# Kernel optimization log

Measured on AMD Instinct MI355X. Metric: run time of the kernel, lower is better.

The kernel has to match this reference:

```python
import jax, jax.numpy as jnp
import numpy as np

B, S, H, D = 2, 2048, 16, 128  # batch, seq, n_head, head_dim; n_embd = H*D
N_EMBD = H * D

def setup_inputs() -> dict:
    key = jax.random.key(0)
    kq, kk, kv = jax.random.split(key, 3)
    q = jax.random.normal(kq, (B, S, H, D), dtype=jnp.float32)
    k = jax.random.normal(kk, (B, S, H, D), dtype=jnp.float32)
    v = jax.random.normal(kv, (B, S, H, D), dtype=jnp.float32)
    return {"q": q, "k": k, "v": v}

def reference(q, k, v):
    # [B,S,H,D] -> [B,H,S,D]
    qh = jnp.transpose(q, (0, 2, 1, 3))
    kh = jnp.transpose(k, (0, 2, 1, 3))
    vh = jnp.transpose(v, (0, 2, 1, 3))
    # scores scaled by head_dim (NOT sqrt), matching the original module
    att = jnp.einsum('bhqd,bhkd->bhqk', qh, kh) / D
    att = jax.nn.softmax(att, axis=-1)
    y = jnp.einsum('bhqk,bhkd->bhqd', att, vh)
    # [B,H,S,D] -> [B,S,H,D] -> [B*S, n_embd]
    y = jnp.transpose(y, (0, 2, 1, 3)).reshape(B * S, N_EMBD)
    return y
```

## Files before the change

### kernel.cpp

```cpp
#include <hip/hip_runtime.h>


#define SEQ   2048
#define NHEAD 16
#define DH    128
#define NB    2
#define BQ    256
#define BK    64
#define NTHR  256
#define KSTR  136
#define VSTR  72
#define NKV   (SEQ / BK)
#define NELEM (NB * SEQ * NHEAD * DH)

typedef __attribute__((ext_vector_type(8)))  short bf16x8;
typedef __attribute__((ext_vector_type(16))) float f32x16;
typedef __attribute__((ext_vector_type(4)))  unsigned int u32x4;

__device__ __forceinline__ unsigned short f2bf(float x) {
    unsigned int u = __builtin_bit_cast(unsigned int, x);
    u += 0x7fffu + ((u >> 16) & 1u);
    return (unsigned short)(u >> 16);
}

__device__ __forceinline__ unsigned int pk2bf(float lo, float hi) {
    return (__builtin_bit_cast(unsigned int, hi) & 0xffff0000u)
         | (__builtin_bit_cast(unsigned int, lo) >> 16);
}

__device__ __forceinline__ void pl32(unsigned int& a, unsigned int& b) {
    asm("v_permlane32_swap_b32 %0, %1" : "+v"(a), "+v"(b));
}

__global__ __launch_bounds__(256) void cvt_bf16(
    const float* __restrict__ q, const float* __restrict__ k,
    const float* __restrict__ v, unsigned short* __restrict__ dst)
{
    const int y = blockIdx.y;
    const float* s = (y == 0) ? q : (y == 1) ? k : v;
    const float scl = (y == 0) ? (1.44269504088896340736f / 128.0f) : 1.0f;
    unsigned short* d = dst + (size_t)y * NELEM;
    const int i = blockIdx.x * 256 + threadIdx.x;
    const float4 x = ((const float4*)s)[i];
    ushort4 o;
    o.x = f2bf(x.x * scl); o.y = f2bf(x.y * scl);
    o.z = f2bf(x.z * scl); o.w = f2bf(x.w * scl);
    ((ushort4*)d)[i] = o;
}

__global__ __launch_bounds__(NTHR, 1) void attn_fwd(
    const unsigned short* __restrict__ Qb,
    const unsigned short* __restrict__ Kb,
    const unsigned short* __restrict__ Vb,
    float* __restrict__ O)
{
    __shared__ unsigned short Kl[2][BK * KSTR];
    __shared__ unsigned short Vl[2][DH * VSTR];

    const int tid  = threadIdx.x;
    const int wave = tid >> 6;
    const int lane = tid & 63;
    const int hx   = lane >> 5;
    const int l32  = lane & 31;

    const int b  = blockIdx.y >> 4;
    const int h  = blockIdx.y & 15;
    const int q0 = blockIdx.x * BQ;

    const size_t rs = (size_t)NHEAD * DH;
    const unsigned short* qb = Qb + (size_t)b * SEQ * rs + (size_t)h * DH;
    const unsigned short* kb = Kb + (size_t)b * SEQ * rs + (size_t)h * DH;
    const unsigned short* vb = Vb + (size_t)b * SEQ * rs + (size_t)h * DH;

    bf16x8 qf[2][8];
    #pragma unroll
    for (int qt = 0; qt < 2; ++qt) {
        const unsigned short* qp =
            qb + (size_t)(q0 + wave * 64 + qt * 32 + l32) * rs + hx * 8;
        #pragma unroll
        for (int c = 0; c < 8; ++c)
            qf[qt][c] = *(const bf16x8*)(qp + c * 16);
    }

    int kgo[4], kls[4];
    #pragma unroll
    for (int p = 0; p < 4; ++p) {
        const int cidx = (wave * 4 + p) * 64 + lane;
        const int key  = cidx >> 4;
        const int cc   = cidx & 15;
        kgo[p] = key * (int)rs + cc * 8;
        kls[p] = key * KSTR + cc * 8;
    }
    const int kp  = tid & 31;
    const int dcv = tid >> 5;

    f32x16 o4[2][4];
    #pragma unroll
    for (int qt = 0; qt < 2; ++qt)
        #pragma unroll
        for (int t = 0; t < 4; ++t)
            #pragma unroll
            for (int r = 0; r < 16; ++r) o4[qt][t][r] = 0.f;
    float lsum[2] = {0.f, 0.f};

    bf16x8 kr[4], vr[4];

    {
        #pragma unroll
        for (int p = 0; p < 4; ++p) kr[p] = *(const bf16x8*)(kb + kgo[p]);
        #pragma unroll
        for (int p = 0; p < 2; ++p) {
            const unsigned short* src = vb + (size_t)(2 * kp) * rs + (dcv + p * 8) * 8;
            vr[p * 2]     = *(const bf16x8*)src;
            vr[p * 2 + 1] = *(const bf16x8*)(src + rs);
        }
        #pragma unroll
        for (int p = 0; p < 4; ++p) *(bf16x8*)&Kl[0][kls[p]] = kr[p];
        unsigned int* vw = (unsigned int*)&Vl[0][0];
        #pragma unroll
        for (int p = 0; p < 2; ++p)
            #pragma unroll
            for (int j = 0; j < 8; ++j) {
                const unsigned int pr = ((unsigned int)(unsigned short)vr[p * 2][j])
                                      | (((unsigned int)(unsigned short)vr[p * 2 + 1][j]) << 16);
                vw[((dcv + p * 8) * 8 + j) * (VSTR / 2) + kp] = pr;
            }
    }
    __syncthreads();

    for (int kv = 0; kv < NKV; ++kv) {
        const int cur = kv & 1;
        const int k0n = ((kv + 1) & (NKV - 1)) * BK;

        #pragma unroll
        for (int p = 0; p < 4; ++p) kr[p] = *(const bf16x8*)(kb + (size_t)k0n * rs + kgo[p]);
        #pragma unroll
        for (int p = 0; p < 2; ++p) {
            const unsigned short* src = vb + (size_t)(k0n + 2 * kp) * rs + (dcv + p * 8) * 8;
            vr[p * 2]     = *(const bf16x8*)src;
            vr[p * 2 + 1] = *(const bf16x8*)(src + rs);
        }

        const unsigned short* Kc = &Kl[cur][0];
        const unsigned short* Vc = &Vl[cur][0];

        #pragma unroll
        for (int kt = 0; kt < 2; ++kt) {
            f32x16 s[2];
            #pragma unroll
            for (int r = 0; r < 16; ++r) { s[0][r] = 0.f; s[1][r] = 0.f; }
            #pragma unroll
            for (int c = 0; c < 8; ++c) {
                bf16x8 kf = *(const bf16x8*)&Kc[(kt * 32 + l32) * KSTR + c * 16 + hx * 8];
                s[0] = __builtin_amdgcn_mfma_f32_32x32x16_bf16(kf, qf[0][c], s[0], 0, 0, 0);
                s[1] = __builtin_amdgcn_mfma_f32_32x32x16_bf16(kf, qf[1][c], s[1], 0, 0, 0);
            }

            unsigned int w[2][4][2];
            #pragma unroll
            for (int qt = 0; qt < 2; ++qt)
                #pragma unroll
                for (int g = 0; g < 4; ++g) {
                    const float e0 = __builtin_amdgcn_exp2f(s[qt][g * 4 + 0]);
                    const float e1 = __builtin_amdgcn_exp2f(s[qt][g * 4 + 1]);
                    const float e2 = __builtin_amdgcn_exp2f(s[qt][g * 4 + 2]);
                    const float e3 = __builtin_amdgcn_exp2f(s[qt][g * 4 + 3]);
                    lsum[qt] += (e0 + e1) + (e2 + e3);
                    w[qt][g][0] = pk2bf(e0, e1);
                    w[qt][g][1] = pk2bf(e2, e3);
                }

            #pragma unroll
            for (int qt = 0; qt < 2; ++qt)
                #pragma unroll
                for (int ks = 0; ks < 2; ++ks) {
                    pl32(w[qt][2 * ks][0], w[qt][2 * ks + 1][0]);
                    pl32(w[qt][2 * ks][1], w[qt][2 * ks + 1][1]);
                }
            bf16x8 pf[2][2];
            #pragma unroll
            for (int qt = 0; qt < 2; ++qt)
                #pragma unroll
                for (int ks = 0; ks < 2; ++ks) {
                    u32x4 t;
                    t.x = w[qt][2 * ks][0];
                    t.y = w[qt][2 * ks][1];
                    t.z = w[qt][2 * ks + 1][0];
                    t.w = w[qt][2 * ks + 1][1];
                    pf[qt][ks] = __builtin_bit_cast(bf16x8, t);
                }

            #pragma unroll
            for (int ks = 0; ks < 2; ++ks)
                #pragma unroll
                for (int dt = 0; dt < 4; ++dt) {
                    bf16x8 vf = *(const bf16x8*)&Vc[(dt * 32 + l32) * VSTR
                                                    + kt * 32 + ks * 16 + hx * 8];
                    o4[0][dt] = __builtin_amdgcn_mfma_f32_32x32x16_bf16(pf[0][ks], vf, o4[0][dt], 0, 0, 0);
                    o4[1][dt] = __builtin_amdgcn_mfma_f32_32x32x16_bf16(pf[1][ks], vf, o4[1][dt], 0, 0, 0);
                }
        }

        const int nxt = cur ^ 1;
        #pragma unroll
        for (int p = 0; p < 4; ++p) *(bf16x8*)&Kl[nxt][kls[p]] = kr[p];
        {
            unsigned int* vw = (unsigned int*)&Vl[nxt][0];
            #pragma unroll
            for (int p = 0; p < 2; ++p)
                #pragma unroll
                for (int j = 0; j < 8; ++j) {
                    const unsigned int pr = ((unsigned int)(unsigned short)vr[p * 2][j])
                                          | (((unsigned int)(unsigned short)vr[p * 2 + 1][j]) << 16);
                    vw[((dcv + p * 8) * 8 + j) * (VSTR / 2) + kp] = pr;
                }
        }
        __syncthreads();
    }

    #pragma unroll
    for (int qt = 0; qt < 2; ++qt) {
        float ls = lsum[qt];
        ls += __shfl_xor(ls, 32, 64);
        const float inv = 1.0f / ls;
        float iv[16];
        #pragma unroll
        for (int r = 0; r < 16; ++r)
            iv[r] = __shfl(inv, (r & 3) + 8 * (r >> 2) + 4 * hx, 64);

        #pragma unroll
        for (int dt = 0; dt < 4; ++dt)
            #pragma unroll
            for (int r = 0; r < 16; ++r) {
                const int ql = (r & 3) + 8 * (r >> 2) + 4 * hx;
                const int qg = q0 + wave * 64 + qt * 32 + ql;
                O[(size_t)(b * SEQ + qg) * rs + (size_t)h * DH + dt * 32 + l32]
                    = o4[qt][dt][r] * iv[r];
            }
    }
}

extern "C" void kernel_launch(void* const* d_in, const int* in_sizes, int n_in,
                              void* d_out, int out_size, void* d_ws, size_t ws_size,
                              hipStream_t stream) {
    const float* q = (const float*)d_in[0];
    const float* k = (const float*)d_in[1];
    const float* v = (const float*)d_in[2];
    float* o = (float*)d_out;
    unsigned short* wsb = (unsigned short*)d_ws;

    cvt_bf16<<<dim3(NELEM / 1024, 3), 256, 0, stream>>>(q, k, v, wsb);
    attn_fwd<<<dim3(SEQ / BQ, NB * NHEAD), dim3(NTHR), 0, stream>>>(
        wsb, wsb + NELEM, wsb + 2 * (size_t)NELEM, o);
}
```

Baseline: 214.5 us.

## Split KV sequence across two thread groups per block and merge via LDS

Doubles the block to 512 threads, with two 256-thread groups each processing half of the key/value tiles for the same query block, using separate double-buffered LDS regions. At the end the partial outputs and row sums are exchanged through shared memory, and each group writes half of the head dimension. The aim is more waves per CU and latency hiding without a max-subtraction rescale, since the softmax has no running max. The cost is extra LDS usage, an epilogue reduction, and higher register pressure under the new launch bounds.

```diff
diff --git a/kernel.cpp b/kernel.cpp
--- a/kernel.cpp
+++ b/kernel.cpp
@@ -7,11 +7,14 @@
 #define NB    2
 #define BQ    256
 #define BK    64
-#define NTHR  256
+#define NTHR  512
 #define KSTR  136
 #define VSTR  72
 #define NKV   (SEQ / BK)
+#define NIT   (NKV / 2)
 #define NELEM (NB * SEQ * NHEAD * DH)
+#define KTILE (BK * KSTR)
+#define VTILE (DH * VSTR)
 
 typedef __attribute__((ext_vector_type(8)))  short bf16x8;
 typedef __attribute__((ext_vector_type(16))) float f32x16;
@@ -48,20 +51,22 @@
     ((ushort4*)d)[i] = o;
 }
 
-__global__ __launch_bounds__(NTHR, 1) void attn_fwd(
+__global__ __launch_bounds__(NTHR, 2) void attn_fwd(
     const unsigned short* __restrict__ Qb,
     const unsigned short* __restrict__ Kb,
     const unsigned short* __restrict__ Vb,
     float* __restrict__ O)
 {
-    __shared__ unsigned short Kl[2][BK * KSTR];
-    __shared__ unsigned short Vl[2][DH * VSTR];
-
-    const int tid  = threadIdx.x;
-    const int wave = tid >> 6;
-    const int lane = tid & 63;
-    const int hx   = lane >> 5;
-    const int l32  = lane & 31;
+    __shared__ unsigned short Sm[4 * KTILE + 4 * VTILE];
+
+    const int tid   = threadIdx.x;
+    const int gt    = tid & 255;
+    const int group = tid >> 8;
+    const int wave  = tid >> 6;
+    const int wv    = wave & 3;
+    const int lane  = tid & 63;
+    const int hx    = lane >> 5;
+    const int l32   = lane & 31;
 
     const int b  = blockIdx.y >> 4;
     const int h  = blockIdx.y & 15;
@@ -76,7 +81,7 @@
     #pragma unroll
     for (int qt = 0; qt < 2; ++qt) {
         const unsigned short* qp =
-            qb + (size_t)(q0 + wave * 64 + qt * 32 + l32) * rs + hx * 8;
+            qb + (size_t)(q0 + wv * 64 + qt * 32 + l32) * rs + hx * 8;
         #pragma unroll
         for (int c = 0; c < 8; ++c)
             qf[qt][c] = *(const bf16x8*)(qp + c * 16);
@@ -85,14 +90,14 @@
     int kgo[4], kls[4];
     #pragma unroll
     for (int p = 0; p < 4; ++p) {
-        const int cidx = (wave * 4 + p) * 64 + lane;
+        const int cidx = (wv * 4 + p) * 64 + lane;
         const int key  = cidx >> 4;
         const int cc   = cidx & 15;
         kgo[p] = key * (int)rs + cc * 8;
         kls[p] = key * KSTR + cc * 8;
     }
-    const int kp  = tid & 31;
-    const int dcv = tid >> 5;
+    const int kp  = gt & 31;
+    const int dcv = gt >> 5;
 
     f32x16 o4[2][4];
     #pragma unroll
@@ -104,19 +109,23 @@
     float lsum[2] = {0.f, 0.f};
 
     bf16x8 kr[4], vr[4];
+    const int t0 = group * NIT;
 
     {
-        #pragma unroll
-        for (int p = 0; p < 4; ++p) kr[p] = *(const bf16x8*)(kb + kgo[p]);
+        const size_t kbase = (size_t)(t0 * BK) * rs;
+        #pragma unroll
+        for (int p = 0; p < 4; ++p) kr[p] = *(const bf16x8*)(kb + kbase + kgo[p]);
         #pragma unroll
         for (int p = 0; p < 2; ++p) {
-            const unsigned short* src = vb + (size_t)(2 * kp) * rs + (dcv + p * 8) * 8;
+            const unsigned short* src =
+                vb + (size_t)(t0 * BK + 2 * kp) * rs + (dcv + p * 8) * 8;
             vr[p * 2]     = *(const bf16x8*)src;
             vr[p * 2 + 1] = *(const bf16x8*)(src + rs);
         }
-        #pragma unroll
-        for (int p = 0; p < 4; ++p) *(bf16x8*)&Kl[0][kls[p]] = kr[p];
-        unsigned int* vw = (unsigned int*)&Vl[0][0];
+        unsigned short* Kw = &Sm[(2 * group + 0) * KTILE];
+        #pragma unroll
+        for (int p = 0; p < 4; ++p) *(bf16x8*)&Kw[kls[p]] = kr[p];
+        unsigned int* vw = (unsigned int*)&Sm[4 * KTILE + (2 * group + 0) * VTILE];
         #pragma unroll
         for (int p = 0; p < 2; ++p)
             #pragma unroll
@@ -128,21 +137,26 @@
     }
     __syncthreads();
 
-    for (int kv = 0; kv < NKV; ++kv) {
-        const int cur = kv & 1;
-        const int k0n = ((kv + 1) & (NKV - 1)) * BK;
-
-        #pragma unroll
-        for (int p = 0; p < 4; ++p) kr[p] = *(const bf16x8*)(kb + (size_t)k0n * rs + kgo[p]);
-        #pragma unroll
-        for (int p = 0; p < 2; ++p) {
-            const unsigned short* src = vb + (size_t)(k0n + 2 * kp) * rs + (dcv + p * 8) * 8;
-            vr[p * 2]     = *(const bf16x8*)src;
-            vr[p * 2 + 1] = *(const bf16x8*)(src + rs);
-        }
-
-        const unsigned short* Kc = &Kl[cur][0];
-        const unsigned short* Vc = &Vl[cur][0];
+    for (int it = 0; it < NIT; ++it) {
+        const int cur   = it & 1;
+        const bool last = (it == NIT - 1);
+        const int k0n   = (t0 + it + 1) * BK;
+
+        if (!last) {
+            #pragma unroll
+            for (int p = 0; p < 4; ++p)
+                kr[p] = *(const bf16x8*)(kb + (size_t)k0n * rs + kgo[p]);
+            #pragma unroll
+            for (int p = 0; p < 2; ++p) {
+                const unsigned short* src =
+                    vb + (size_t)(k0n + 2 * kp) * rs + (dcv + p * 8) * 8;
+                vr[p * 2]     = *(const bf16x8*)src;
+                vr[p * 2 + 1] = *(const bf16x8*)(src + rs);
+            }
+        }
+
+        const unsigned short* Kc = &Sm[(2 * group + cur) * KTILE];
+        const unsigned short* Vc = &Sm[4 * KTILE + (2 * group + cur) * VTILE];
 
         #pragma unroll
         for (int kt = 0; kt < 2; ++kt) {
@@ -201,11 +215,12 @@
                 }
         }
 
-        const int nxt = cur ^ 1;
-        #pragma unroll
-        for (int p = 0; p < 4; ++p) *(bf16x8*)&Kl[nxt][kls[p]] = kr[p];
-        {
-            unsigned int* vw = (unsigned int*)&Vl[nxt][0];
+        if (!last) {
+            const int nxt = cur ^ 1;
+            unsigned short* Kw = &Sm[(2 * group + nxt) * KTILE];
+            #pragma unroll
+            for (int p = 0; p < 4; ++p) *(bf16x8*)&Kw[kls[p]] = kr[p];
+            unsigned int* vw = (unsigned int*)&Sm[4 * KTILE + (2 * group + nxt) * VTILE];
             #pragma unroll
             for (int p = 0; p < 2; ++p)
                 #pragma unroll
@@ -218,25 +233,77 @@
         __syncthreads();
     }
 
+    float lsc[2];
     #pragma unroll
     for (int qt = 0; qt < 2; ++qt) {
         float ls = lsum[qt];
         ls += __shfl_xor(ls, 32, 64);
-        const float inv = 1.0f / ls;
+        lsc[qt] = ls;
+    }
+
+    float* Ep = (float*)Sm;
+    float* mine = Ep + (size_t)((group << 8) + gt) * 68;
+
+    if (group == 0) {
+        #pragma unroll
+        for (int j = 0; j < 4; ++j) {
+            float4 a, bq, c, d;
+            a.x  = o4[0][2][4*j+0]; a.y  = o4[0][2][4*j+1]; a.z  = o4[0][2][4*j+2]; a.w  = o4[0][2][4*j+3];
+            bq.x = o4[0][3][4*j+0]; bq.y = o4[0][3][4*j+1]; bq.z = o4[0][3][4*j+2]; bq.w = o4[0][3][4*j+3];
+            c.x  = o4[1][2][4*j+0]; c.y  = o4[1][2][4*j+1]; c.z  = o4[1][2][4*j+2]; c.w  = o4[1][2][4*j+3];
+            d.x  = o4[1][3][4*j+0]; d.y  = o4[1][3][4*j+1]; d.z  = o4[1][3][4*j+2]; d.w  = o4[1][3][4*j+3];
+            *(float4*)&mine[ 0 + 4*j] = a;
+            *(float4*)&mine[16 + 4*j] = bq;
+            *(float4*)&mine[32 + 4*j] = c;
+            *(float4*)&mine[48 + 4*j] = d;
+        }
+    } else {
+        #pragma unroll
+        for (int j = 0; j < 4; ++j) {
+            float4 a, bq, c, d;
+            a.x  = o4[0][0][4*j+0]; a.y  = o4[0][0][4*j+1]; a.z  = o4[0][0][4*j+2]; a.w  = o4[0][0][4*j+3];
+            bq.x = o4[0][1][4*j+0]; bq.y = o4[0][1][4*j+1]; bq.z = o4[0][1][4*j+2]; bq.w = o4[0][1][4*j+3];
+            c.x  = o4[1][0][4*j+0]; c.y  = o4[1][0][4*j+1]; c.z  = o4[1][0][4*j+2]; c.w  = o4[1][0][4*j+3];
+            d.x  = o4[1][1][4*j+0]; d.y  = o4[1][1][4*j+1]; d.z  = o4[1][1][4*j+2]; d.w  = o4[1][1][4*j+3];
+            *(float4*)&mine[ 0 + 4*j] = a;
+            *(float4*)&mine[16 + 4*j] = bq;
+            *(float4*)&mine[32 + 4*j] = c;
+            *(float4*)&mine[48 + 4*j] = d;
+        }
+    }
+    mine[64] = lsc[0];
+    mine[65] = lsc[1];
+    __syncthreads();
+
+    const float* peer = Ep + (size_t)(((1 - group) << 8) + gt) * 68;
+    #pragma unroll
+    for (int qt = 0; qt < 2; ++qt) {
+        const float lt  = lsc[qt] + peer[64 + qt];
+        const float inv = 1.0f / lt;
         float iv[16];
         #pragma unroll
         for (int r = 0; r < 16; ++r)
             iv[r] = __shfl(inv, (r & 3) + 8 * (r >> 2) + 4 * hx, 64);
 
-        #pragma unroll
-        for (int dt = 0; dt < 4; ++dt)
+        if (group == 0) {
             #pragma unroll
             for (int r = 0; r < 16; ++r) {
                 const int ql = (r & 3) + 8 * (r >> 2) + 4 * hx;
-                const int qg = q0 + wave * 64 + qt * 32 + ql;
-                O[(size_t)(b * SEQ + qg) * rs + (size_t)h * DH + dt * 32 + l32]
-                    = o4[qt][dt][r] * iv[r];
-            }
+                float* orow = O + (size_t)(b * SEQ + q0 + wv * 64 + qt * 32 + ql) * rs
+                                + (size_t)h * DH + l32;
+                orow[ 0] = (o4[qt][0][r] + peer[(qt * 2 + 0) * 16 + r]) * iv[r];
+                orow[32] = (o4[qt][1][r] + peer[(qt * 2 + 1) * 16 + r]) * iv[r];
+            }
+        } else {
+            #pragma unroll
+            for (int r = 0; r < 16; ++r) {
+                const int ql = (r & 3) + 8 * (r >> 2) + 4 * hx;
+                float* orow = O + (size_t)(b * SEQ + q0 + wv * 64 + qt * 32 + ql) * rs
+                                + (size_t)h * DH + l32;
+                orow[64] = (o4[qt][2][r] + peer[(qt * 2 + 0) * 16 + r]) * iv[r];
+                orow[96] = (o4[qt][3][r] + peer[(qt * 2 + 1) * 16 + r]) * iv[r];
+            }
+        }
     }
 }
 
```

New measurement: 303.2 us. +41.3%, slower.
